# Optimization experiments

Measured on AMD Instinct MI355X. Metric: run time of the kernel, lower is better.

Reference implementation:

```python
import jax, jax.numpy as jnp
import numpy as np

C_TOKEN, C_PAIR, N_HEADS, C_S = 768, 128, 16, 384
C_HID = C_TOKEN // N_HEADS
EPS = 1e-5


def _ln(x):
    # LayerNorm without affine params
    m = jnp.mean(x, axis=-1, keepdims=True)
    v = jnp.mean(jnp.square(x - m), axis=-1, keepdims=True)
    return (x - m) * jax.lax.rsqrt(v + EPS)


def setup_inputs() -> dict:
    key = jax.random.key(0)
    ks = jax.random.split(key, 16)
    B, N = 2, 768
    std = 0.02
    inp = {
        "a": jax.random.normal(ks[0], (B, N, C_TOKEN), jnp.float32),
        "s": jax.random.normal(ks[1], (B, N, C_S), jnp.float32),
        "z": jax.random.normal(ks[2], (B, N, N, C_PAIR), jnp.float32),
        "bias_mask": jax.random.normal(ks[3], (B, N, N), jnp.float32),
        # AdaLN conditioning projections
        "Wg_ada": jax.random.normal(ks[4], (C_S, C_TOKEN), jnp.float32) * std,
        "bg_ada": jnp.zeros((C_TOKEN,), jnp.float32),
        "Wb_ada": jax.random.normal(ks[5], (C_S, C_TOKEN), jnp.float32) * std,
        # QKV
        "Wq": jax.random.normal(ks[6], (C_TOKEN, C_TOKEN), jnp.float32) * std,
        "bq": jnp.zeros((C_TOKEN,), jnp.float32),
        "Wk": jax.random.normal(ks[7], (C_TOKEN, C_TOKEN), jnp.float32) * std,
        "Wv": jax.random.normal(ks[8], (C_TOKEN, C_TOKEN), jnp.float32) * std,
        # pair bias
        "Wpb": jax.random.normal(ks[9], (C_PAIR, N_HEADS), jnp.float32) * std,
        "pn_gamma": jnp.ones((C_PAIR,), jnp.float32),
        "pn_beta": jnp.zeros((C_PAIR,), jnp.float32),
        # gating / output
        "Wgate": jax.random.normal(ks[10], (C_TOKEN, C_TOKEN), jnp.float32) * std,
        "Wout": jax.random.normal(ks[11], (C_TOKEN, C_TOKEN), jnp.float32) * std,
        "Wog": jax.random.normal(ks[12], (C_S, C_TOKEN), jnp.float32) * std,
        "bog": jnp.full((C_TOKEN,), -2.0, jnp.float32),  # adaLN-Zero init
    }
    return inp


def reference(a, s, z, bias_mask, Wg_ada, bg_ada, Wb_ada, Wq, bq, Wk, Wv,
              Wpb, pn_gamma, pn_beta, Wgate, Wout, Wog, bog):
    B, N, _ = a.shape
    # Adaptive LayerNorm: a_ln modulated by conditioning s (AF3 Alg 26)
    a_ln = _ln(a)
    s_ln = _ln(s)
    a_norm = jax.nn.sigmoid(s_ln @ Wg_ada + bg_ada) * a_ln + s_ln @ Wb_ada
    # QKV projections -> [B, H, N, D]
    def split_heads(x):
        return x.reshape(B, N, N_HEADS, C_HID).transpose(0, 2, 1, 3)
    q = split_heads(a_norm @ Wq + bq)
    k = split_heads(a_norm @ Wk)
    v = split_heads(a_norm @ Wv)
    # Pair bias: LayerNorm(z) -> per-head bias [B, H, N, N]
    z_ln = _ln(z) * pn_gamma + pn_beta
    pair_bias = jnp.einsum('bijc,ch->bhij', z_ln, Wpb)
    pair_bias = pair_bias + bias_mask[:, None, :, :]
    # Attention
    logits = jnp.einsum('bhqd,bhkd->bhqk', q, k) / np.float32(np.sqrt(C_HID))
    attn = jax.nn.softmax(logits + pair_bias, axis=-1)
    g = jax.nn.sigmoid(split_heads(a_norm @ Wgate))
    o = g * jnp.einsum('bhqk,bhkd->bhqd', attn, v)  # gated attention output
    o = o.transpose(0, 2, 1, 3).reshape(B, N, C_TOKEN)
    out = o @ Wout
    # Adaptive output gating from raw conditioning s
    out = jax.nn.sigmoid(s @ Wog + bog) * out
    return out
```

## Files before the change

kernel.cpp:

```cpp
#include <hip/hip_runtime.h>
#include <math.h>
#include <stdint.h>

namespace {
constexpr int kN = 768, kCT = 768, kCS = 384, kCP = 128, kNH = 16, kHD = 48;
constexpr float kEps = 1e-5f;
constexpr float kQScale = 0.14433756729740643f;
}

typedef __attribute__((ext_vector_type(8))) short short8;
typedef __attribute__((ext_vector_type(4))) float floatx4;

__device__ __forceinline__ float sigf(float x) { return 1.f / (1.f + expf(-x)); }
__device__ __forceinline__ unsigned short f2bf(float x) {
  uint32_t v = __builtin_bit_cast(uint32_t, x);
  return (unsigned short)((v + 0x7fffu + ((v >> 16) & 1u)) >> 16);
}
__device__ __forceinline__ float bf2f(unsigned short u) {
  uint32_t v = ((uint32_t)u) << 16;
  return __builtin_bit_cast(float, v);
}

#if __has_builtin(__builtin_amdgcn_global_load_lds)
#define HAVE_GLL 1
#define ASYNC_COPY16(gp, lp)                                                     \
  __builtin_amdgcn_global_load_lds((const __attribute__((address_space(1))) void*)(gp), \
                                   (__attribute__((address_space(3))) void*)(lp), 16, 0, 0)
#else
#define HAVE_GLL 0
#endif

__global__ __launch_bounds__(256) void transpose_pack_kernel(
    const float* __restrict__ Wg, const float* __restrict__ Wb,
    const float* __restrict__ Wq, const float* __restrict__ Wk,
    const float* __restrict__ Wv, const float* __restrict__ Wgate,
    const float* __restrict__ Wog, const float* __restrict__ Wout,
    unsigned short* __restrict__ p_adaT, unsigned short* __restrict__ p_qkvT,
    unsigned short* __restrict__ WogT, unsigned short* __restrict__ WoutT) {
  __shared__ float tile[32][33];
  const int cum[8] = {288, 576, 1152, 1728, 2304, 2880, 3168, 3744};
  const int srcK[8] = {384, 384, 768, 768, 768, 768, 384, 768};
  int bid = blockIdx.x;
  int m = 0;
#pragma unroll
  for (int q = 0; q < 8; ++q)
    if (bid >= cum[q]) m = q + 1;
  const int base = m ? cum[m - 1] : 0;
  const int tloc = bid - base;
  const float* src = m == 0 ? Wg : m == 1 ? Wb : m == 2 ? Wq : m == 3 ? Wk
                   : m == 4 ? Wv : m == 5 ? Wgate : m == 6 ? Wog : Wout;
  unsigned short* dst =
      m == 0 ? p_adaT : m == 1 ? (p_adaT + 768 * 384)
    : m == 2 ? p_qkvT : m == 3 ? (p_qkvT + 768 * 768)
    : m == 4 ? (p_qkvT + 2 * 768 * 768) : m == 5 ? (p_qkvT + 3 * 768 * 768)
    : m == 6 ? WogT : WoutT;
  const int K = srcK[m];
  const int bk = tloc / 24, bn = tloc % 24;
  const int k0 = bk * 32, n0 = bn * 32;
  const int tx = threadIdx.x & 31, ty = threadIdx.x >> 5;
#pragma unroll
  for (int r = 0; r < 4; ++r)
    tile[ty + 8 * r][tx] = src[(size_t)(k0 + ty + 8 * r) * 768 + n0 + tx];
  __syncthreads();
#pragma unroll
  for (int r = 0; r < 4; ++r)
    dst[(size_t)(n0 + ty + 8 * r) * K + k0 + tx] = f2bf(tile[tx][ty + 8 * r]);
}

__global__ __launch_bounds__(256) void pack_kernel(
    const float* __restrict__ bg, const float* __restrict__ bq,
    const float* __restrict__ s, const float* __restrict__ Wpb,
    const float* __restrict__ gamma, const float* __restrict__ beta,
    float* __restrict__ pb_ada, float* __restrict__ pb_qk,
    unsigned short* __restrict__ s_bf, float* __restrict__ gamW,
    float* __restrict__ pairC) {
  const int T1 = 1536;
  const int T2 = T1 + 3072;
  const int T3 = T2 + 1536 * 384;
  const int T4 = T3 + 2048;
  const int T5 = T4 + 32;
  int idx = blockIdx.x * 256 + threadIdx.x;
  if (idx < T1) {
    pb_ada[idx] = (idx < 768) ? bg[idx] : 0.f;
  } else if (idx < T2) {
    int c = idx - T1;
    pb_qk[c] = (c < 768) ? bq[c] : 0.f;
  } else if (idx < T3) {
    int r = idx - T2;
    s_bf[r] = f2bf(s[r]);
  } else if (idx < T4) {
    int r = idx - T3;
    int c = r >> 4, h = r & 15;
    gamW[r] = gamma[c] * Wpb[c * 16 + h];
  } else if (idx < T5) {
    int r = idx - T4;
    float acc = 0.f;
    if (r < 16) {
      for (int c = 0; c < 128; ++c) acc += beta[c] * Wpb[c * 16 + r];
      pairC[r] = acc;
    } else {
      int h = r - 16;
      for (int c = 0; c < 128; ++c) acc += gamma[c] * Wpb[c * 16 + h];
      pairC[r] = acc;
    }
  }
}

template <int C>
__global__ __launch_bounds__(256) void ln_kernel(const float* __restrict__ x,
                                                 float* __restrict__ y) {
  constexpr int NV = (C + 255) / 256;
  const int row = blockIdx.x;
  const float* xr = x + (size_t)row * C;
  float vals[NV];
  float s = 0.f, ss = 0.f;
#pragma unroll
  for (int it = 0; it < NV; ++it) {
    int c = threadIdx.x + it * 256;
    float v = (c < C) ? xr[c] : 0.f;
    vals[it] = v;
    s += v;
    ss = fmaf(v, v, ss);
  }
#pragma unroll
  for (int m = 1; m < 64; m <<= 1) { s += __shfl_xor(s, m); ss += __shfl_xor(ss, m); }
  __shared__ float red[8];
  __shared__ float mb[2];
  const int wid = threadIdx.x >> 6, lane = threadIdx.x & 63;
  if (lane == 0) { red[wid * 2] = s; red[wid * 2 + 1] = ss; }
  __syncthreads();
  if (threadIdx.x == 0) {
    float S = red[0] + red[2] + red[4] + red[6];
    float SS = red[1] + red[3] + red[5] + red[7];
    float mean = S / C;
    float var = SS / C - mean * mean;
    mb[0] = mean;
    mb[1] = rsqrtf(var + kEps);
  }
  __syncthreads();
  const float mean = mb[0], rs = mb[1];
#pragma unroll
  for (int it = 0; it < NV; ++it) {
    int c = threadIdx.x + it * 256;
    if (c < C) y[(size_t)row * C + c] = (vals[it] - mean) * rs;
  }
}

template <int C>
__global__ __launch_bounds__(256) void ln_bf_kernel(const float* __restrict__ x,
                                                    unsigned short* __restrict__ y) {
  constexpr int NV = (C + 255) / 256;
  const int row = blockIdx.x;
  const float* xr = x + (size_t)row * C;
  float vals[NV];
  float s = 0.f, ss = 0.f;
#pragma unroll
  for (int it = 0; it < NV; ++it) {
    int c = threadIdx.x + it * 256;
    float v = (c < C) ? xr[c] : 0.f;
    vals[it] = v;
    s += v;
    ss = fmaf(v, v, ss);
  }
#pragma unroll
  for (int m = 1; m < 64; m <<= 1) { s += __shfl_xor(s, m); ss += __shfl_xor(ss, m); }
  __shared__ float red[8];
  __shared__ float mb[2];
  const int wid = threadIdx.x >> 6, lane = threadIdx.x & 63;
  if (lane == 0) { red[wid * 2] = s; red[wid * 2 + 1] = ss; }
  __syncthreads();
  if (threadIdx.x == 0) {
    float S = red[0] + red[2] + red[4] + red[6];
    float SS = red[1] + red[3] + red[5] + red[7];
    float mean = S / C;
    float var = SS / C - mean * mean;
    mb[0] = mean;
    mb[1] = rsqrtf(var + kEps);
  }
  __syncthreads();
  const float mean = mb[0], rs = mb[1];
#pragma unroll
  for (int it = 0; it < NV; ++it) {
    int c = threadIdx.x + it * 256;
    if (c < C) y[(size_t)row * C + c] = f2bf((vals[it] - mean) * rs);
  }
}

__global__ __launch_bounds__(256) void anorm_kernel(const float* __restrict__ gb,
                                                    const float* __restrict__ a_ln,
                                                    unsigned short* __restrict__ a_norm) {
  int idx = blockIdx.x * 256 + threadIdx.x;
  int row = idx / kCT, col = idx % kCT;
  float g = gb[(size_t)row * (2 * kCT) + col];
  float bv = gb[(size_t)row * (2 * kCT) + kCT + col];
  a_norm[idx] = f2bf(sigf(g) * a_ln[idx] + bv);
}

template <int BM>
__global__ __launch_bounds__(256) void gemm_bf_kernel(
    const unsigned short* __restrict__ A, const unsigned short* __restrict__ Wt,
    const float* __restrict__ bias, const float* __restrict__ aux,
    float* __restrict__ C, int M, int Nn, int K, int sig_start) {
  constexpr int TM = BM / 32;
  __shared__ __align__(16) unsigned short As[BM * 32];
  __shared__ __align__(16) unsigned short Bs[128 * 32];
  const int t = threadIdx.x;
  const int wid = t >> 6, lane = t & 63;
  const int quad = lane >> 4, m16 = lane & 15;
  const int wm = (wid >> 1) * (BM / 2), wn = (wid & 1) * 64;
  const int bm = blockIdx.y * BM, bn = blockIdx.x * 128;
  const int swz = quad ^ ((m16 >> 1) & 3);
  const int ci0 = t, ci1 = t + 256;
  const int am0 = ci0 >> 2, ak0 = ((ci0 & 3) ^ ((am0 >> 1) & 3)) * 8;
  const int am1 = ci1 >> 2, ak1 = ((ci1 & 3) ^ ((am1 >> 1) & 3)) * 8;
  const unsigned short* ga0 = A + (size_t)(bm + am0) * K + ak0;
  const unsigned short* ga1 = A + (size_t)(bm + am1) * K + ak1;
  const unsigned short* gw0 = Wt + (size_t)(bn + am0) * K + ak0;
  const unsigned short* gw1 = Wt + (size_t)(bn + am1) * K + ak1;
  floatx4 acc[TM][4] = {};
  for (int k0 = 0; k0 < K; k0 += 32) {
    __syncthreads();
#if HAVE_GLL
    ASYNC_COPY16(ga0 + k0, &As[ci0 * 8]);
    if constexpr (BM == 128) ASYNC_COPY16(ga1 + k0, &As[ci1 * 8]);
    ASYNC_COPY16(gw0 + k0, &Bs[ci0 * 8]);
    ASYNC_COPY16(gw1 + k0, &Bs[ci1 * 8]);
#else
    short8 ra0 = *(const short8*)(ga0 + k0);
    short8 rw0 = *(const short8*)(gw0 + k0);
    short8 rw1 = *(const short8*)(gw1 + k0);
    *(short8*)&As[ci0 * 8] = ra0;
    if constexpr (BM == 128) {
      short8 ra1 = *(const short8*)(ga1 + k0);
      *(short8*)&As[ci1 * 8] = ra1;
    }
    *(short8*)&Bs[ci0 * 8] = rw0;
    *(short8*)&Bs[ci1 * 8] = rw1;
#endif
    __syncthreads();
    short8 af[TM], bfv[4];
#pragma unroll
    for (int tm = 0; tm < TM; ++tm)
      af[tm] = *(const short8*)&As[(wm + tm * 16 + m16) * 32 + swz * 8];
#pragma unroll
    for (int tn = 0; tn < 4; ++tn)
      bfv[tn] = *(const short8*)&Bs[(wn + tn * 16 + m16) * 32 + swz * 8];
#pragma unroll
    for (int tm = 0; tm < TM; ++tm)
#pragma unroll
      for (int tn = 0; tn < 4; ++tn)
        acc[tm][tn] = __builtin_amdgcn_mfma_f32_16x16x32_bf16(af[tm], bfv[tn], acc[tm][tn], 0, 0, 0);
  }
#pragma unroll
  for (int tm = 0; tm < TM; ++tm) {
    const int row0 = bm + wm + tm * 16 + quad * 4;
#pragma unroll
    for (int tn = 0; tn < 4; ++tn) {
      const int col = bn + wn + tn * 16 + m16;
      const float badd = bias ? bias[col] : 0.f;
#pragma unroll
      for (int r = 0; r < 4; ++r) {
        float v = acc[tm][tn][r] + badd;
        if (col >= sig_start) v = sigf(v);
        if (aux) v *= aux[(size_t)(row0 + r) * Nn + col];
        C[(size_t)(row0 + r) * Nn + col] = v;
      }
    }
  }
}

__global__ __launch_bounds__(256) void pairbias2_kernel(
    const float* __restrict__ z, const float* __restrict__ mask,
    const float* __restrict__ gamW, const float* __restrict__ pairC,
    unsigned short* __restrict__ pb) {
  const int t = threadIdx.x;
  const int b = blockIdx.z, i = blockIdx.y;
  const int j = blockIdx.x * 256 + t;
  const float4* __restrict__ zr = (const float4*)&z[((size_t)(b * kN + i) * kN + j) * kCP];
  const float4* __restrict__ gw = (const float4*)gamW;
  float sum = 0.f, ss = 0.f;
  floatx4 acc[4] = {};
#pragma unroll 4
  for (int c4 = 0; c4 < 32; ++c4) {
    const float4 v = zr[c4];
#pragma unroll
    for (int u = 0; u < 4; ++u) {
      const float vv = (u == 0) ? v.x : (u == 1) ? v.y : (u == 2) ? v.z : v.w;
      sum += vv;
      ss = fmaf(vv, vv, ss);
      const int c = c4 * 4 + u;
#pragma unroll
      for (int q = 0; q < 4; ++q) {
        const float4 g = gw[c * 4 + q];
        acc[q][0] = fmaf(vv, g.x, acc[q][0]);
        acc[q][1] = fmaf(vv, g.y, acc[q][1]);
        acc[q][2] = fmaf(vv, g.z, acc[q][2]);
        acc[q][3] = fmaf(vv, g.w, acc[q][3]);
      }
    }
  }
  const float mean = sum * (1.f / 128.f);
  const float var = ss * (1.f / 128.f) - mean * mean;
  const float rs = rsqrtf(var + kEps);
  const float mk = mask[(size_t)(b * kN + i) * kN + j];
  const size_t pbase = ((size_t)(b * kNH) * kN + i) * kN + j;
#pragma unroll
  for (int h = 0; h < 16; ++h) {
    const float a = acc[h >> 2][h & 3];
    const float res = fmaf(rs, fmaf(-mean, pairC[16 + h], a), pairC[h]) + mk;
    pb[pbase + (size_t)h * kN * kN] = f2bf(res);
  }
}

__global__ __launch_bounds__(1024) void attn_kernel(
    const float* __restrict__ qkvg, const unsigned short* __restrict__ pb,
    unsigned short* __restrict__ o_out) {
  __shared__ float kt[64 * 52];
  __shared__ float vt[64 * 52];
  __shared__ float qs[16][48];
  const int b = blockIdx.z, h = blockIdx.y;
  const int t = threadIdx.x, wid = t >> 6, lane = t & 63;
  const int i = blockIdx.x * 16 + wid;
  const size_t rowi = (size_t)(b * kN + i) * (4 * kCT);
  if (lane < 12) {
    float4 q4 = *(const float4*)&qkvg[rowi + h * kHD + lane * 4];
    qs[wid][lane * 4 + 0] = q4.x * kQScale;
    qs[wid][lane * 4 + 1] = q4.y * kQScale;
    qs[wid][lane * 4 + 2] = q4.z * kQScale;
    qs[wid][lane * 4 + 3] = q4.w * kQScale;
  }
  const int jl = t / 12, d4 = t % 12;
  const bool loader = (t < 768);
  float4 kreg, vreg;
  if (loader) {
    const size_t rowj = (size_t)(b * kN + jl) * (4 * kCT);
    kreg = *(const float4*)&qkvg[rowj + kCT + h * kHD + d4 * 4];
    vreg = *(const float4*)&qkvg[rowj + 2 * kCT + h * kHD + d4 * 4];
  }
  float o[48];
#pragma unroll
  for (int d = 0; d < 48; ++d) o[d] = 0.f;
  float mrun = -INFINITY, lsum = 0.f;
  const unsigned short* pbrow = &pb[((size_t)(b * kNH + h) * kN + i) * kN];
  for (int c = 0; c < 12; ++c) {
    __syncthreads();
    if (loader) {
      *(float4*)&kt[jl * 52 + d4 * 4] = kreg;
      *(float4*)&vt[jl * 52 + d4 * 4] = vreg;
    }
    __syncthreads();
    if (loader && c < 11) {
      const size_t rowj = (size_t)(b * kN + (c + 1) * 64 + jl) * (4 * kCT);
      kreg = *(const float4*)&qkvg[rowj + kCT + h * kHD + d4 * 4];
      vreg = *(const float4*)&qkvg[rowj + 2 * kCT + h * kHD + d4 * 4];
    }
    float l0 = bf2f(pbrow[c * 64 + lane]), l1 = 0.f, l2 = 0.f, l3 = 0.f;
#pragma unroll
    for (int d4i = 0; d4i < 12; ++d4i) {
      float4 kk = *(const float4*)&kt[lane * 52 + d4i * 4];
      float4 qq = *(const float4*)&qs[wid][d4i * 4];
      l0 = fmaf(qq.x, kk.x, l0);
      l1 = fmaf(qq.y, kk.y, l1);
      l2 = fmaf(qq.z, kk.z, l2);
      l3 = fmaf(qq.w, kk.w, l3);
    }
    float logit = (l0 + l1) + (l2 + l3);
    float mx = logit;
#pragma unroll
    for (int m = 1; m < 64; m <<= 1) mx = fmaxf(mx, __shfl_xor(mx, m));
    const float mnew = fmaxf(mrun, mx);
    const float alpha = expf(mrun - mnew);
    const float p = expf(logit - mnew);
    lsum = fmaf(lsum, alpha, p);
#pragma unroll
    for (int d4i = 0; d4i < 12; ++d4i) {
      float4 vv = *(const float4*)&vt[lane * 52 + d4i * 4];
      o[d4i * 4 + 0] = fmaf(o[d4i * 4 + 0], alpha, p * vv.x);
      o[d4i * 4 + 1] = fmaf(o[d4i * 4 + 1], alpha, p * vv.y);
      o[d4i * 4 + 2] = fmaf(o[d4i * 4 + 2], alpha, p * vv.z);
      o[d4i * 4 + 3] = fmaf(o[d4i * 4 + 3], alpha, p * vv.w);
    }
    mrun = mnew;
  }
#pragma unroll
  for (int m = 1; m < 64; m <<= 1) lsum += __shfl_xor(lsum, m);
#pragma unroll
  for (int d = 0; d < 48; ++d) {
#pragma unroll
    for (int m = 1; m < 64; m <<= 1) o[d] += __shfl_xor(o[d], m);
  }
  if (lane == 0) {
    const float inv = 1.f / lsum;
    unsigned short* orow = o_out + (size_t)(b * kN + i) * kCT + h * kHD;
#pragma unroll
    for (int d4i = 0; d4i < 12; ++d4i) {
      float4 g4 = *(const float4*)&qkvg[rowi + 3 * kCT + h * kHD + d4i * 4];
      uint32_t u0 = (uint32_t)f2bf(g4.x * o[d4i * 4 + 0] * inv) |
                    ((uint32_t)f2bf(g4.y * o[d4i * 4 + 1] * inv) << 16);
      uint32_t u1 = (uint32_t)f2bf(g4.z * o[d4i * 4 + 2] * inv) |
                    ((uint32_t)f2bf(g4.w * o[d4i * 4 + 3] * inv) << 16);
      *(uint32_t*)&orow[d4i * 4 + 0] = u0;
      *(uint32_t*)&orow[d4i * 4 + 2] = u1;
    }
  }
}

extern "C" void kernel_launch(void* const* d_in, const int* in_sizes, int n_in,
                              void* d_out, int out_size, void* d_ws, size_t ws_size,
                              hipStream_t stream) {
  const float* a      = (const float*)d_in[0];
  const float* s      = (const float*)d_in[1];
  const float* z      = (const float*)d_in[2];
  const float* mask   = (const float*)d_in[3];
  const float* Wg_ada = (const float*)d_in[4];
  const float* bg_ada = (const float*)d_in[5];
  const float* Wb_ada = (const float*)d_in[6];
  const float* Wq     = (const float*)d_in[7];
  const float* bq     = (const float*)d_in[8];
  const float* Wk     = (const float*)d_in[9];
  const float* Wv     = (const float*)d_in[10];
  const float* Wpb    = (const float*)d_in[11];
  const float* pn_g   = (const float*)d_in[12];
  const float* pn_b   = (const float*)d_in[13];
  const float* Wgate  = (const float*)d_in[14];
  const float* Wout   = (const float*)d_in[15];
  const float* Wog    = (const float*)d_in[16];
  const float* bog    = (const float*)d_in[17];
  float* out = (float*)d_out;

  char* p = (char*)d_ws;
  auto alloc = [&](size_t bytes) -> char* {
    char* r = p;
    p += (bytes + 255) & ~(size_t)255;
    return r;
  };
  float* a_ln  = (float*)alloc((size_t)1536 * 768 * 4);
  float* gb    = (float*)alloc((size_t)1536 * 1536 * 4);
  float* qkvg  = (float*)alloc((size_t)1536 * 3072 * 4);
  float* ogate = (float*)alloc((size_t)1536 * 768 * 4);
  unsigned short* s_ln   = (unsigned short*)alloc((size_t)1536 * 384 * 2);
  unsigned short* a_nrm  = (unsigned short*)alloc((size_t)1536 * 768 * 2);
  unsigned short* s_bf   = (unsigned short*)alloc((size_t)1536 * 384 * 2);
  unsigned short* o_g    = (unsigned short*)alloc((size_t)1536 * 768 * 2);
  unsigned short* pbias  = (unsigned short*)alloc((size_t)2 * 16 * 768 * 768 * 2);
  unsigned short* p_adaT = (unsigned short*)alloc((size_t)1536 * 384 * 2);
  unsigned short* p_qkvT = (unsigned short*)alloc((size_t)3072 * 768 * 2);
  unsigned short* WogT   = (unsigned short*)alloc((size_t)768 * 384 * 2);
  unsigned short* WoutT  = (unsigned short*)alloc((size_t)768 * 768 * 2);
  float* pb_ada = (float*)alloc(1536 * 4);
  float* pb_qk  = (float*)alloc(3072 * 4);
  float* gamW   = (float*)alloc(2048 * 4);
  float* pairC  = (float*)alloc(32 * 4);

  transpose_pack_kernel<<<dim3(3744), 256, 0, stream>>>(
      Wg_ada, Wb_ada, Wq, Wk, Wv, Wgate, Wog, Wout, p_adaT, p_qkvT, WogT, WoutT);
  const int packTot = 1536 + 3072 + 1536 * 384 + 2048 + 32;
  pack_kernel<<<dim3((packTot + 255) / 256), 256, 0, stream>>>(
      bg_ada, bq, s, Wpb, pn_g, pn_b, pb_ada, pb_qk, s_bf, gamW, pairC);
  ln_kernel<768><<<dim3(1536), 256, 0, stream>>>(a, a_ln);
  ln_bf_kernel<384><<<dim3(1536), 256, 0, stream>>>(s, s_ln);
  gemm_bf_kernel<64><<<dim3(12, 24), 256, 0, stream>>>(
      s_ln, p_adaT, pb_ada, nullptr, gb, 1536, 1536, 384, 1 << 30);
  anorm_kernel<<<dim3(1536 * 768 / 256), 256, 0, stream>>>(gb, a_ln, a_nrm);
  gemm_bf_kernel<128><<<dim3(24, 12), 256, 0, stream>>>(
      a_nrm, p_qkvT, pb_qk, nullptr, qkvg, 1536, 3072, 768, 2304);
  gemm_bf_kernel<64><<<dim3(6, 24), 256, 0, stream>>>(
      s_bf, WogT, bog, nullptr, ogate, 1536, 768, 384, 0);
  pairbias2_kernel<<<dim3(3, 768, 2), 256, 0, stream>>>(z, mask, gamW, pairC, pbias);
  attn_kernel<<<dim3(48, 16, 2), 1024, 0, stream>>>(qkvg, pbias, o_g);
  gemm_bf_kernel<64><<<dim3(6, 24), 256, 0, stream>>>(
      o_g, WoutT, nullptr, ogate, out, 1536, 768, 768, 1 << 30);
}
```

Baseline: 1.206 ms.

## Compute pair-bias projection with bf16 MFMA over LDS-staged z tiles

The pair-bias kernel is rewritten so each block stages 128 rows of z as bf16 in LDS, with two threads per row computing partial LayerNorm statistics. The 128x16 projection is then done with 16x16x32 bf16 MFMA instructions instead of per-thread scalar FMAs, using a transposed bf16 copy of gamma*Wpb. Global loads of z are split across two threads per row, which changes the access pattern. The intent is to cut the ALU cost of the projection in this z-bandwidth-bound kernel, at the cost of rounding z and the weights to bf16 before the dot product.

```diff
diff --git a/kernel.cpp b/kernel.cpp
--- a/kernel.cpp
+++ b/kernel.cpp
@@ -72,7 +72,7 @@
     const float* __restrict__ s, const float* __restrict__ Wpb,
     const float* __restrict__ gamma, const float* __restrict__ beta,
     float* __restrict__ pb_ada, float* __restrict__ pb_qk,
-    unsigned short* __restrict__ s_bf, float* __restrict__ gamW,
+    unsigned short* __restrict__ s_bf, unsigned short* __restrict__ gamWT,
     float* __restrict__ pairC) {
   const int T1 = 1536;
   const int T2 = T1 + 3072;
@@ -90,8 +90,8 @@
     s_bf[r] = f2bf(s[r]);
   } else if (idx < T4) {
     int r = idx - T3;
-    int c = r >> 4, h = r & 15;
-    gamW[r] = gamma[c] * Wpb[c * 16 + h];
+    int h = r >> 7, c = r & 127;
+    gamWT[r] = f2bf(gamma[c] * Wpb[c * 16 + h]);
   } else if (idx < T5) {
     int r = idx - T4;
     float acc = 0.f;
@@ -269,46 +269,82 @@
   }
 }
 
-__global__ __launch_bounds__(256) void pairbias2_kernel(
+__global__ __launch_bounds__(256, 4) void pairbias3_kernel(
     const float* __restrict__ z, const float* __restrict__ mask,
-    const float* __restrict__ gamW, const float* __restrict__ pairC,
+    const unsigned short* __restrict__ gamWT, const float* __restrict__ pairC,
     unsigned short* __restrict__ pb) {
+  __shared__ __align__(16) unsigned short zbf[128 * 136];
+  __shared__ float2 pstat[256];
+  __shared__ float2 mstat[128];
   const int t = threadIdx.x;
+  const int jj = t & 127, half = t >> 7;
   const int b = blockIdx.z, i = blockIdx.y;
-  const int j = blockIdx.x * 256 + t;
-  const float4* __restrict__ zr = (const float4*)&z[((size_t)(b * kN + i) * kN + j) * kCP];
-  const float4* __restrict__ gw = (const float4*)gamW;
+  const int j0 = blockIdx.x * 128;
+  const float* zrow = &z[((size_t)(b * kN + i) * kN + j0 + jj) * kCP + half * 64];
   float sum = 0.f, ss = 0.f;
-  floatx4 acc[4] = {};
-#pragma unroll 4
-  for (int c4 = 0; c4 < 32; ++c4) {
-    const float4 v = zr[c4];
-#pragma unroll
-    for (int u = 0; u < 4; ++u) {
-      const float vv = (u == 0) ? v.x : (u == 1) ? v.y : (u == 2) ? v.z : v.w;
-      sum += vv;
-      ss = fmaf(vv, vv, ss);
-      const int c = c4 * 4 + u;
-#pragma unroll
-      for (int q = 0; q < 4; ++q) {
-        const float4 g = gw[c * 4 + q];
-        acc[q][0] = fmaf(vv, g.x, acc[q][0]);
-        acc[q][1] = fmaf(vv, g.y, acc[q][1]);
-        acc[q][2] = fmaf(vv, g.z, acc[q][2]);
-        acc[q][3] = fmaf(vv, g.w, acc[q][3]);
-      }
-    }
-  }
-  const float mean = sum * (1.f / 128.f);
-  const float var = ss * (1.f / 128.f) - mean * mean;
-  const float rs = rsqrtf(var + kEps);
-  const float mk = mask[(size_t)(b * kN + i) * kN + j];
-  const size_t pbase = ((size_t)(b * kNH) * kN + i) * kN + j;
-#pragma unroll
-  for (int h = 0; h < 16; ++h) {
-    const float a = acc[h >> 2][h & 3];
-    const float res = fmaf(rs, fmaf(-mean, pairC[16 + h], a), pairC[h]) + mk;
-    pb[pbase + (size_t)h * kN * kN] = f2bf(res);
+#pragma unroll
+  for (int g = 0; g < 2; ++g) {
+    float4 v[8];
+#pragma unroll
+    for (int u = 0; u < 8; ++u) v[u] = ((const float4*)zrow)[g * 8 + u];
+#pragma unroll
+    for (int u = 0; u < 8; ++u) {
+      sum += (v[u].x + v[u].y) + (v[u].z + v[u].w);
+      ss = fmaf(v[u].x, v[u].x, ss);
+      ss = fmaf(v[u].y, v[u].y, ss);
+      ss = fmaf(v[u].z, v[u].z, ss);
+      ss = fmaf(v[u].w, v[u].w, ss);
+    }
+#pragma unroll
+    for (int k = 0; k < 4; ++k) {
+      short8 pk;
+      const float4 a = v[2 * k], bb = v[2 * k + 1];
+      pk[0] = (short)f2bf(a.x); pk[1] = (short)f2bf(a.y);
+      pk[2] = (short)f2bf(a.z); pk[3] = (short)f2bf(a.w);
+      pk[4] = (short)f2bf(bb.x); pk[5] = (short)f2bf(bb.y);
+      pk[6] = (short)f2bf(bb.z); pk[7] = (short)f2bf(bb.w);
+      const int c16 = half * 8 + g * 4 + k;
+      *(short8*)&zbf[(jj * 17 + c16) * 8] = pk;
+    }
+  }
+  pstat[t] = make_float2(sum, ss);
+  __syncthreads();
+  if (t < 128) {
+    const float S = pstat[t].x + pstat[t + 128].x;
+    const float SS = pstat[t].y + pstat[t + 128].y;
+    const float mean = S * (1.f / 128.f);
+    const float var = SS * (1.f / 128.f) - mean * mean;
+    mstat[t] = make_float2(mean, rsqrtf(var + kEps));
+  }
+  __syncthreads();
+  const int wid = t >> 6, lane = t & 63;
+  const int m16 = lane & 15, quad = lane >> 4;
+  short8 ga[4];
+#pragma unroll
+  for (int kk = 0; kk < 4; ++kk)
+    ga[kk] = *(const short8*)&gamWT[m16 * 128 + kk * 32 + quad * 8];
+  const float4 cb = ((const float4*)pairC)[quad];
+  const float4 gs = ((const float4*)pairC)[4 + quad];
+#pragma unroll
+  for (int u = 0; u < 2; ++u) {
+    const int tt = wid * 2 + u;
+    const int jloc = tt * 16 + m16;
+    floatx4 acc = {};
+#pragma unroll
+    for (int kk = 0; kk < 4; ++kk) {
+      const short8 bf = *(const short8*)&zbf[(jloc * 17 + kk * 4 + quad) * 8];
+      acc = __builtin_amdgcn_mfma_f32_16x16x32_bf16(ga[kk], bf, acc, 0, 0, 0);
+    }
+    const float mean = mstat[jloc].x, rs = mstat[jloc].y;
+    const float mk = mask[(size_t)(b * kN + i) * kN + j0 + jloc];
+    const size_t obase = ((size_t)(b * kNH + quad * 4) * kN + i) * kN + j0 + jloc;
+#pragma unroll
+    for (int r = 0; r < 4; ++r) {
+      const float gsr = r == 0 ? gs.x : r == 1 ? gs.y : r == 2 ? gs.z : gs.w;
+      const float cbr = r == 0 ? cb.x : r == 1 ? cb.y : r == 2 ? cb.z : cb.w;
+      const float res = fmaf(rs, fmaf(-mean, gsr, acc[r]), cbr) + mk;
+      pb[obase + (size_t)r * kN * kN] = f2bf(res);
+    }
   }
 }
 
@@ -447,16 +483,16 @@
   unsigned short* p_qkvT = (unsigned short*)alloc((size_t)3072 * 768 * 2);
   unsigned short* WogT   = (unsigned short*)alloc((size_t)768 * 384 * 2);
   unsigned short* WoutT  = (unsigned short*)alloc((size_t)768 * 768 * 2);
+  unsigned short* gamWT  = (unsigned short*)alloc(2048 * 2);
   float* pb_ada = (float*)alloc(1536 * 4);
   float* pb_qk  = (float*)alloc(3072 * 4);
-  float* gamW   = (float*)alloc(2048 * 4);
   float* pairC  = (float*)alloc(32 * 4);
 
   transpose_pack_kernel<<<dim3(3744), 256, 0, stream>>>(
       Wg_ada, Wb_ada, Wq, Wk, Wv, Wgate, Wog, Wout, p_adaT, p_qkvT, WogT, WoutT);
   const int packTot = 1536 + 3072 + 1536 * 384 + 2048 + 32;
   pack_kernel<<<dim3((packTot + 255) / 256), 256, 0, stream>>>(
-      bg_ada, bq, s, Wpb, pn_g, pn_b, pb_ada, pb_qk, s_bf, gamW, pairC);
+      bg_ada, bq, s, Wpb, pn_g, pn_b, pb_ada, pb_qk, s_bf, gamWT, pairC);
   ln_kernel<768><<<dim3(1536), 256, 0, stream>>>(a, a_ln);
   ln_bf_kernel<384><<<dim3(1536), 256, 0, stream>>>(s, s_ln);
   gemm_bf_kernel<64><<<dim3(12, 24), 256, 0, stream>>>(
@@ -466,7 +502,7 @@
       a_nrm, p_qkvT, pb_qk, nullptr, qkvg, 1536, 3072, 768, 2304);
   gemm_bf_kernel<64><<<dim3(6, 24), 256, 0, stream>>>(
       s_bf, WogT, bog, nullptr, ogate, 1536, 768, 384, 0);
-  pairbias2_kernel<<<dim3(3, 768, 2), 256, 0, stream>>>(z, mask, gamW, pairC, pbias);
+  pairbias3_kernel<<<dim3(6, 768, 2), 256, 0, stream>>>(z, mask, gamWT, pairC, pbias);
   attn_kernel<<<dim3(48, 16, 2), 1024, 0, stream>>>(qkvg, pbias, o_g);
   gemm_bf_kernel<64><<<dim3(6, 24), 256, 0, stream>>>(
       o_g, WoutT, nullptr, ogate, out, 1536, 768, 768, 1 << 30);
```

After: 1.211 ms. About the same (+0.4%).
